# Performance work log

Hardware: AMD Instinct MI355X
Metric: run time of the kernel (lower is better)

The kernel has to match this reference:

```python
import jax, jax.numpy as jnp
import numpy as np
from jax import lax

N = 20000        # nodes
E = 320000       # directed edges (avg degree 16)
F_IN = 512       # input feature dim
HID = 64         # hidden_layer
K_NEI = 8        # sampled neighbors per node
L = K_NEI + 1    # local subgraph size (self + neighbors)
N_TPL = 10       # N_templates
NT = 8           # N_templates_nodes
N_CLS = 6
ALPHA = 0.5      # FGW trade-off
EPS = 0.1        # entropic regularization
N_OUTER = 3      # outer CG iterations
N_SINK = 5       # sinkhorn iterations per outer step


def setup_inputs() -> dict:
    rng = np.random.default_rng(0)
    src = rng.integers(0, N, E).astype(np.int64)
    dst = rng.integers(0, N, E).astype(np.int64)
    edge_index = np.stack([src, dst])

    # fixed-size neighbor table (pad with self, mask)
    nbr = np.full((N, K_NEI), -1, np.int64)
    cnt = np.zeros(N, np.int64)
    for s, d in zip(src, dst):
        c = cnt[s]
        if c < K_NEI:
            nbr[s, c] = d
            cnt[s] = c + 1
    pad = nbr < 0
    self_col = np.arange(N, dtype=np.int64)
    nbr = np.where(pad, self_col[:, None], nbr)
    nbr_mask = np.concatenate([np.ones((N, 1)), (~pad).astype(np.float64)], 1).astype(np.float32)

    # local adjacency among {self, neighbors}: [N, L, L]
    idx_full = np.concatenate([self_col[:, None], nbr], 1)  # [N, L]
    edge_keys = np.unique(src * N + dst)
    keys = idx_full[:, :, None] * N + idx_full[:, None, :]
    C_local = np.isin(keys, edge_keys).astype(np.float32)

    ks = jax.random.split(jax.random.key(0), 10)
    x = jax.random.normal(ks[0], (N, F_IN), jnp.float32)
    W1 = jax.random.normal(ks[1], (F_IN, HID), jnp.float32) / np.float32(np.sqrt(F_IN))
    b1 = jnp.zeros((HID,), jnp.float32)
    W2 = jax.random.normal(ks[2], (HID, HID), jnp.float32) / np.float32(np.sqrt(HID))
    b2 = jnp.zeros((HID,), jnp.float32)
    t = jax.random.uniform(ks[3], (N_TPL, NT, NT), jnp.float32)
    templates = 0.5 * (t + jnp.swapaxes(t, 1, 2))  # symmetric template adjacency
    templates_features = jax.random.normal(ks[4], (N_TPL, NT, HID), jnp.float32)
    Wlin = jax.random.normal(ks[5], (HID + N_TPL, N_CLS), jnp.float32) / np.float32(np.sqrt(HID + N_TPL))
    blin = jnp.zeros((N_CLS,), jnp.float32)
    return {"x": x, "edge_index": jnp.asarray(edge_index), "nbr_idx": jnp.asarray(nbr),
            "nbr_mask": jnp.asarray(nbr_mask), "C_local": jnp.asarray(C_local),
            "W1": W1, "b1": b1, "W2": W2, "b2": b2,
            "templates": templates, "templates_features": templates_features,
            "Wlin": Wlin, "blin": blin}


def gcn(x, W, b, src, dst, n):
    xw = x @ W
    sl = jnp.arange(n)
    s = jnp.concatenate([src, sl])
    d = jnp.concatenate([dst, sl])
    deg = jax.ops.segment_sum(jnp.ones_like(s, jnp.float32), d, num_segments=n)
    dinv = lax.rsqrt(deg)
    coef = dinv[s] * dinv[d]
    return jax.ops.segment_sum(xw[s] * coef[:, None], d, num_segments=n) + b


def fgw_dist(M, C1, h1, C2, h2):
    # entropic fused GW (square loss) with fixed iterations; padded rows have h1 = 0
    f1 = C1 * C1
    f2 = C2 * C2
    constC = (f1 @ h1)[:, None] + (f2 @ h2)[None, :]
    T0 = h1[:, None] * h2[None, :]

    def outer(T, _):
        tens = constC - 2.0 * (C1 @ T @ C2)
        G = (1.0 - ALPHA) * M + ALPHA * tens
        Kmat = jnp.exp(-G / EPS)

        def sink(carry, _):
            u, v = carry
            u = h1 / (Kmat @ v + 1e-16)
            v = h2 / (Kmat.T @ u + 1e-16)
            return (u, v), None

        (u, v), _ = lax.scan(sink, (jnp.ones_like(h1), jnp.ones_like(h2)), None, length=N_SINK)
        return u[:, None] * Kmat * v[None, :], None

    T, _ = lax.scan(outer, T0, None, length=N_OUTER)
    tens = constC - 2.0 * (C1 @ T @ C2)
    return jnp.sum(T * ((1.0 - ALPHA) * M + ALPHA * tens))


def distance_to_template(x, nbr_idx, nbr_mask, C_local, templates_features, templates):
    n = x.shape[0]
    idx_full = jnp.concatenate([jnp.arange(n)[:, None], nbr_idx], axis=1)  # [N, L]
    xl = x[idx_full]  # [N, L, HID]
    # squared euclidean cost to each template: [N, T, L, NT]
    inner = jnp.einsum('nld,tmd->ntlm', xl, templates_features)
    M = (jnp.sum(xl * xl, -1)[:, None, :, None]
         + jnp.sum(templates_features * templates_features, -1)[None, :, None, :]
         - 2.0 * inner)
    h1 = nbr_mask / jnp.sum(nbr_mask, -1, keepdims=True)  # [N, L]
    h2 = jnp.full((NT,), 1.0 / NT, jnp.float32)

    per_tpl = jax.vmap(fgw_dist, in_axes=(0, None, None, 0, None))
    per_node = jax.vmap(per_tpl, in_axes=(0, 0, 0, None, None))
    return per_node(M, C_local, h1, templates, h2)  # [N, N_TPL]


def reference(x, edge_index, nbr_idx, nbr_mask, C_local, W1, b1, W2, b2,
              templates, templates_features, Wlin, blin):
    src, dst = edge_index[0], edge_index[1]
    n = x.shape[0]
    h = jax.nn.relu(gcn(x, W1, b1, src, dst, n))
    h = gcn(h, W2, b2, src, dst, n)
    y = distance_to_template(h, nbr_idx, nbr_mask, C_local, templates_features, templates)
    out = jnp.concatenate([h, y], axis=1) @ Wlin + blin
    return jax.nn.relu(out)
```

## Files before the change

kernel.cpp:

```cpp
#include <hip/hip_runtime.h>


#define NN   20000
#define EE   320000
#define FIN  512
#define HID  64
#define KNEI 8
#define LSZ  9
#define NTPL 10
#define NTN  8
#define NCLS 6
#define CAP  48

typedef unsigned short bf16_t;
typedef unsigned short us8 __attribute__((ext_vector_type(8)));

__device__ __forceinline__ float b2f(bf16_t u) {
  union { unsigned int i; float f; } v; v.i = ((unsigned int)u) << 16; return v.f;
}
__device__ __forceinline__ bf16_t f2b(float f) {
  union { float f; unsigned int i; } v; v.f = f;
  unsigned int x = v.i;
  return (bf16_t)((x + 0x7fffu + ((x >> 16) & 1u)) >> 16);
}
__device__ __forceinline__ float ldf(const void* p, long i, int fp32) {
  return fp32 ? ((const float*)p)[i] : b2f(((const bf16_t*)p)[i]);
}
__device__ __forceinline__ int ldi(const void* p, long i, int i64) {
  return i64 ? (int)((const long long*)p)[i] : ((const int*)p)[i];
}
__device__ __forceinline__ float frcp(float x) { return __builtin_amdgcn_rcpf(x); }

__global__ __launch_bounds__(128) void probe_kernel(const void* __restrict__ x,
                                                    const void* __restrict__ ei,
                                                    const void* __restrict__ tfeat,
                                                    int* __restrict__ flags,
                                                    float* __restrict__ tn2min) {
  __shared__ int sfl[2];
  __shared__ float tn2s[80];
  int tid = threadIdx.x;
  if (tid == 0) {
    int sane = 0;
    for (int k = 0; k < 64; k += 2) {
      bf16_t u = ((const bf16_t*)x)[k];
      int e = (u >> 7) & 0xff;
      if (e >= 112 && e <= 142) sane++;
    }
    int f0 = (sane < 24) ? 1 : 0;
    int zc = 0;
    for (int k = 1; k < 64; k += 2)
      if (((const int*)ei)[k] == 0) zc++;
    int f1 = (zc >= 16) ? 1 : 0;
    flags[0] = f0; flags[1] = f1;
    sfl[0] = f0; sfl[1] = f1;
  }
  __syncthreads();
  if (tid < 80) {
    int fF = sfl[0];
    float s = 0.f;
    for (int k = 0; k < HID; ++k) {
      float v = ldf(tfeat, (long)tid * HID + k, fF);
      s += v * v;
    }
    tn2s[tid] = s;
  }
  __syncthreads();
  if (tid == 0) {
    float gmin = 1e30f;
    for (int t = 0; t < NTPL; ++t) {
      float m = tn2s[t * 8];
      for (int r = 1; r < 8; ++r) m = fminf(m, tn2s[t * 8 + r]);
      tn2min[t] = m;
      gmin = fminf(gmin, m);
    }
    tn2min[NTPL] = gmin;
  }
}

__global__ __launch_bounds__(256) void hist_kernel(const void* __restrict__ ei,
                                                   int* __restrict__ cnt,
                                                   const int* __restrict__ flags) {
  int i = blockIdx.x * 256 + threadIdx.x;
  if (i < EE) atomicAdd(&cnt[ldi(ei, (long)EE + i, flags[1])], 1);
}
__global__ __launch_bounds__(256) void dinv_kernel(const int* __restrict__ cnt,
                                                   float* __restrict__ dinv) {
  int i = blockIdx.x * 256 + threadIdx.x;
  if (i < NN) dinv[i] = rsqrtf((float)cnt[i] + 1.0f);
}

__global__ __launch_bounds__(256) void scatter_kernel(const void* __restrict__ ei,
                                                      int* __restrict__ pos,
                                                      int* __restrict__ slot,
                                                      const int* __restrict__ flags) {
  int i = blockIdx.x * 256 + threadIdx.x;
  if (i >= EE) return;
  int i64 = flags[1];
  int s = ldi(ei, i, i64);
  int d = ldi(ei, (long)EE + i, i64);
  int p = atomicAdd(&pos[d], 1);
  if (p < CAP) slot[d * CAP + p] = s;
}

__global__ __launch_bounds__(256) void gemm1_kernel(const void* __restrict__ x,
                                                    const void* __restrict__ W1,
                                                    float* __restrict__ xw1,
                                                    const int* __restrict__ flags) {
  int wave = blockIdx.x * 4 + (threadIdx.x >> 6);
  int lane = threadIdx.x & 63;
  int row0 = wave * 4;
  if (row0 >= NN) return;
  float a0 = 0.f, a1 = 0.f, a2 = 0.f, a3 = 0.f;
  if (!flags[0]) {
    const bf16_t* xb = (const bf16_t*)x + (long)row0 * FIN;
    const bf16_t* wp = (const bf16_t*)W1;
#pragma unroll 2
    for (int k8 = 0; k8 < FIN / 8; ++k8) {
      us8 r0 = *(const us8*)(xb + k8 * 8);
      us8 r1 = *(const us8*)(xb + FIN + k8 * 8);
      us8 r2 = *(const us8*)(xb + 2 * FIN + k8 * 8);
      us8 r3 = *(const us8*)(xb + 3 * FIN + k8 * 8);
#pragma unroll
      for (int q = 0; q < 8; ++q) {
        float w = b2f(wp[(k8 * 8 + q) * HID + lane]);
        a0 += b2f(r0[q]) * w;
        a1 += b2f(r1[q]) * w;
        a2 += b2f(r2[q]) * w;
        a3 += b2f(r3[q]) * w;
      }
    }
  } else {
    const float* x0 = (const float*)x + (long)row0 * FIN;
    const float* wp = (const float*)W1;
#pragma unroll 8
    for (int k = 0; k < FIN; ++k) {
      float w = wp[k * HID + lane];
      a0 += x0[k] * w;
      a1 += x0[FIN + k] * w;
      a2 += x0[2 * FIN + k] * w;
      a3 += x0[3 * FIN + k] * w;
    }
  }
  xw1[(long)(row0 + 0) * HID + lane] = a0;
  xw1[(long)(row0 + 1) * HID + lane] = a1;
  xw1[(long)(row0 + 2) * HID + lane] = a2;
  xw1[(long)(row0 + 3) * HID + lane] = a3;
}

__global__ __launch_bounds__(256) void gemm2_kernel(const float* __restrict__ h,
                                                    const void* __restrict__ W2,
                                                    float* __restrict__ xw2,
                                                    const int* __restrict__ flags) {
  int wave = blockIdx.x * 4 + (threadIdx.x >> 6);
  int lane = threadIdx.x & 63;
  int row0 = wave * 4;
  if (row0 >= NN) return;
  int fF = flags[0];
  float a0 = 0.f, a1 = 0.f, a2 = 0.f, a3 = 0.f;
  const float* h0 = h + (long)row0 * HID;
#pragma unroll 4
  for (int k4 = 0; k4 < HID / 4; ++k4) {
    float4 r0 = *(const float4*)(h0 + k4 * 4);
    float4 r1 = *(const float4*)(h0 + HID + k4 * 4);
    float4 r2 = *(const float4*)(h0 + 2 * HID + k4 * 4);
    float4 r3 = *(const float4*)(h0 + 3 * HID + k4 * 4);
#pragma unroll
    for (int q = 0; q < 4; ++q) {
      float w = ldf(W2, (k4 * 4 + q) * HID + lane, fF);
      float e0 = (q == 0) ? r0.x : (q == 1) ? r0.y : (q == 2) ? r0.z : r0.w;
      float e1 = (q == 0) ? r1.x : (q == 1) ? r1.y : (q == 2) ? r1.z : r1.w;
      float e2 = (q == 0) ? r2.x : (q == 1) ? r2.y : (q == 2) ? r2.z : r2.w;
      float e3 = (q == 0) ? r3.x : (q == 1) ? r3.y : (q == 2) ? r3.z : r3.w;
      a0 += e0 * w; a1 += e1 * w; a2 += e2 * w; a3 += e3 * w;
    }
  }
  xw2[(long)(row0 + 0) * HID + lane] = a0;
  xw2[(long)(row0 + 1) * HID + lane] = a1;
  xw2[(long)(row0 + 2) * HID + lane] = a2;
  xw2[(long)(row0 + 3) * HID + lane] = a3;
}

__global__ __launch_bounds__(256) void gather_kernel(const float* __restrict__ xw,
                                                     const float* __restrict__ dinv,
                                                     const int* __restrict__ cnt,
                                                     const int* __restrict__ slot,
                                                     float* __restrict__ h,
                                                     const void* __restrict__ bias,
                                                     const int* __restrict__ flags,
                                                     int relu_bias) {
  int n = blockIdx.x * 4 + (threadIdx.x >> 6);
  if (n >= NN) return;
  int c = threadIdx.x & 63;
  float dn = dinv[n];
  float acc = xw[(long)n * HID + c] * dn;
  int m = cnt[n]; if (m > CAP) m = CAP;
  const int* sl = slot + (long)n * CAP;
  int sN = (m > 0) ? sl[0] : 0;
  for (int e = 0; e < m; ++e) {
    int s = sN;
    if (e + 1 < m) sN = sl[e + 1];
    acc += xw[(long)s * HID + c] * dinv[s];
  }
  acc *= dn;
  if (relu_bias) {
    acc += ldf(bias, c, flags[0]);
    acc = acc > 0.f ? acc : 0.f;
  }
  h[(long)n * HID + c] = acc;
}

__global__ __launch_bounds__(256) void norms_kernel(const float* __restrict__ h2,
                                                    const void* __restrict__ b2v,
                                                    float* __restrict__ n2,
                                                    const int* __restrict__ flags) {
  int n = blockIdx.x * 4 + (threadIdx.x >> 6);
  if (n >= NN) return;
  int c = threadIdx.x & 63;
  float v = h2[(long)n * HID + c] + ldf(b2v, c, flags[0]);
  float s = v * v;
  s += __shfl_xor(s, 1); s += __shfl_xor(s, 2); s += __shfl_xor(s, 4);
  s += __shfl_xor(s, 8); s += __shfl_xor(s, 16); s += __shfl_xor(s, 32);
  if (c == 0) n2[n] = s;
}

#define NODES_PB 4
#define TPN 80
#define XLP 65

__global__ __launch_bounds__(320, 2) void fgw_kernel(
    const float* __restrict__ h2,
    const void* __restrict__ b2v,
    const void* __restrict__ nbr_idx,
    const void* __restrict__ nbr_mask,
    const void* __restrict__ C_local,
    const void* __restrict__ tmpl,
    const void* __restrict__ tfeat,
    const void* __restrict__ Wlin,
    const void* __restrict__ blin,
    void* __restrict__ out,
    const int* __restrict__ flags,
    const float* __restrict__ tn2min,
    const float* __restrict__ n2)
{
  const int tid = threadIdx.x;
  const int fF = flags[0];
  const int fI = flags[1];
  const int nb = tid / TPN;
  const int local = tid - nb * TPN;
  const int t = local >> 3;
  const int j = local & 7;
  const int n = blockIdx.x * NODES_PB + nb;
  const int lane = tid & 63;
  const int ob = lane & 56;

  __shared__ float xlS[NODES_PB][LSZ][XLP];
  __shared__ float C1S[NODES_PB][81];
  __shared__ float hwS[NODES_PB][LSZ];
  __shared__ float f1S[NODES_PB][LSZ];
  __shared__ float xnS[NODES_PB][LSZ];
  __shared__ float distS[NODES_PB][NTPL];
  __shared__ float xmaxS[NODES_PB];
  __shared__ int   needS[NODES_PB];
  __shared__ int   sidxS[NODES_PB][LSZ];

  if (local < LSZ) {
    int idx = (local == 0) ? n : ldi(nbr_idx, (long)n * KNEI + local - 1, fI);
    sidxS[nb][local] = idx;
    xnS[nb][local] = n2[idx];
  }
  if (local < HID)
    xlS[nb][0][local] = h2[(long)n * HID + local] + ldf(b2v, local, fF);
  __syncthreads();

  if (local == 0) {
    float xm = xnS[nb][0];
#pragma unroll
    for (int l = 1; l < LSZ; ++l) xm = fmaxf(xm, xnS[nb][l]);
    xmaxS[nb] = xm;
    needS[nb] = ((sqrtf(tn2min[NTPL]) - sqrtf(xm)) >= 5.0990195f) ? 0 : 1;
  }
  __syncthreads();

  const int need = needS[nb];
  if (need) {
    for (int i = local; i < 8 * HID; i += TPN) {
      int l = 1 + (i >> 6), k = i & 63;
      xlS[nb][l][k] = h2[(long)sidxS[nb][l] * HID + k] + ldf(b2v, k, fF);
    }
    for (int i = local; i < 81; i += TPN)
      C1S[nb][i] = ldf(C_local, (long)n * 81 + i, fF);
  }
  __syncthreads();

  if (need && local < LSZ) {
    int l = local;
    float msum = 0.f, f1 = 0.f;
#pragma unroll
    for (int jj = 0; jj < LSZ; ++jj) {
      float mj = ldf(nbr_mask, (long)n * LSZ + jj, fF);
      msum += mj;
      float c = C1S[nb][l * LSZ + jj];
      f1 += c * c * mj;
    }
    float inv = frcp(msum);
    hwS[nb][l] = ldf(nbr_mask, (long)n * LSZ + l, fF) * inv;
    f1S[nb][l] = f1 * inv;
  }
  __syncthreads();

  bool slow = need && ((sqrtf(tn2min[t]) - sqrtf(xmaxS[nb])) < 5.0990195f);
  if (slow) {
    float C2c[NTN];
    float f2h2;
    {
      float s = 0.f;
#pragma unroll
      for (int m = 0; m < NTN; ++m) {
        C2c[m] = ldf(tmpl, t * 64 + m * 8 + j, fF);
        float r = ldf(tmpl, t * 64 + j * 8 + m, fF);
        s += r * r;
      }
      f2h2 = s * 0.125f;
    }
    float hwr[LSZ], f1r[LSZ];
#pragma unroll
    for (int l = 0; l < LSZ; ++l) { hwr[l] = hwS[nb][l]; f1r[l] = f1S[nb][l]; }

    float Mc[LSZ];
    {
      float accI[LSZ];
#pragma unroll
      for (int l = 0; l < LSZ; ++l) accI[l] = 0.f;
      float tn2 = 0.f;
      const long tb = (long)local * HID;
      for (int kb = 0; kb < 8; ++kb) {
        float r[8];
#pragma unroll
        for (int q = 0; q < 8; ++q) r[q] = ldf(tfeat, tb + kb * 8 + q, fF);
#pragma unroll
        for (int q = 0; q < 8; ++q) tn2 += r[q] * r[q];
#pragma unroll
        for (int l = 0; l < LSZ; ++l) {
          float s = 0.f;
#pragma unroll
          for (int q = 0; q < 8; ++q) s += xlS[nb][l][kb * 8 + q] * r[q];
          accI[l] += s;
        }
      }
#pragma unroll
      for (int l = 0; l < LSZ; ++l)
        Mc[l] = xnS[nb][l] + tn2 - 2.f * accI[l];
    }

    float Tc[LSZ], Kc[LSZ], u[LSZ];
#pragma unroll
    for (int l = 0; l < LSZ; ++l) Tc[l] = hwr[l] * 0.125f;

    float v = 1.0f;
    for (int outer = 0; outer < 3; ++outer) {
      float Ac[LSZ];
#pragma unroll
      for (int l = 0; l < LSZ; ++l) {
        float s = 0.f;
#pragma unroll
        for (int l2 = 0; l2 < LSZ; ++l2) s += C1S[nb][l * LSZ + l2] * Tc[l2];
        Ac[l] = s;
      }
#pragma unroll
      for (int l = 0; l < LSZ; ++l) {
        float s = 0.f;
#pragma unroll
        for (int m = 0; m < NTN; ++m) s += __shfl(Ac[l], ob + m) * C2c[m];
        float tens = f1r[l] + f2h2 - 2.f * s;
        Kc[l] = __expf(-5.0f * (Mc[l] + tens));
      }
      v = 1.0f;
      for (int it = 0; it < 5; ++it) {
#pragma unroll
        for (int l = 0; l < LSZ; ++l) {
          float p = Kc[l] * v;
          p += __shfl_xor(p, 1); p += __shfl_xor(p, 2); p += __shfl_xor(p, 4);
          u[l] = hwr[l] * frcp(p + 1e-16f);
        }
        float s = 0.f;
#pragma unroll
        for (int l = 0; l < LSZ; ++l) s += Kc[l] * u[l];
        v = 0.125f * frcp(s + 1e-16f);
      }
#pragma unroll
      for (int l = 0; l < LSZ; ++l) Tc[l] = u[l] * Kc[l] * v;
    }
    {
      float Ac[LSZ];
#pragma unroll
      for (int l = 0; l < LSZ; ++l) {
        float s = 0.f;
#pragma unroll
        for (int l2 = 0; l2 < LSZ; ++l2) s += C1S[nb][l * LSZ + l2] * Tc[l2];
        Ac[l] = s;
      }
      float cl = 0.f;
#pragma unroll
      for (int l = 0; l < LSZ; ++l) {
        float s = 0.f;
#pragma unroll
        for (int m = 0; m < NTN; ++m) s += __shfl(Ac[l], ob + m) * C2c[m];
        float tens = f1r[l] + f2h2 - 2.f * s;
        cl += Tc[l] * 0.5f * (Mc[l] + tens);
      }
      cl += __shfl_xor(cl, 1); cl += __shfl_xor(cl, 2); cl += __shfl_xor(cl, 4);
      if (j == 0) distS[nb][t] = cl;
    }
  } else if (j == 0) {
    distS[nb][t] = 0.f;
  }
  __syncthreads();

  if (local < NCLS) {
    int c = local;
    float acc = ldf(blin, c, fF);
#pragma unroll
    for (int k = 0; k < HID; ++k)
      acc += xlS[nb][0][k] * ldf(Wlin, k * NCLS + c, fF);
#pragma unroll
    for (int tt = 0; tt < NTPL; ++tt)
      acc += distS[nb][tt] * ldf(Wlin, (HID + tt) * NCLS + c, fF);
    float r = acc > 0.f ? acc : 0.f;
    if (fF) ((float*)out)[(long)n * NCLS + c] = r;
    else    ((bf16_t*)out)[(long)n * NCLS + c] = f2b(r);
  }
}

extern "C" void kernel_launch(void* const* d_in, const int* in_sizes, int n_in,
                              void* d_out, int out_size, void* d_ws, size_t ws_size,
                              hipStream_t stream) {
  (void)in_sizes; (void)n_in; (void)out_size; (void)ws_size;
  const void* x     = d_in[0];
  const void* ei    = d_in[1];
  const void* nbr   = d_in[2];
  const void* nmask = d_in[3];
  const void* Cl    = d_in[4];
  const void* W1    = d_in[5];
  const void* b1    = d_in[6];
  const void* W2    = d_in[7];
  const void* b2    = d_in[8];
  const void* tmpl  = d_in[9];
  const void* tfeat = d_in[10];
  const void* Wlin  = d_in[11];
  const void* blin  = d_in[12];

  int*   flags  = (int*)d_ws;
  float* tn2min = (float*)d_ws + 4;
  float* dinv   = (float*)d_ws + 16;
  float* n2     = dinv + NN;
  int*   cnt    = (int*)(n2 + NN);
  int*   pos    = cnt + NN;
  int*   slot   = pos + NN;
  float* bufA   = (float*)(slot + (long)CAP * NN);
  float* bufB   = bufA + (long)NN * HID;

  probe_kernel<<<1, 128, 0, stream>>>(x, ei, tfeat, flags, tn2min);

  hipMemsetAsync(cnt, 0, NN * sizeof(int), stream);
  hipMemsetAsync(pos, 0, NN * sizeof(int), stream);
  hist_kernel<<<(EE + 255) / 256, 256, 0, stream>>>(ei, cnt, flags);
  dinv_kernel<<<(NN + 255) / 256, 256, 0, stream>>>(cnt, dinv);
  scatter_kernel<<<(EE + 255) / 256, 256, 0, stream>>>(ei, pos, slot, flags);

  gemm1_kernel<<<NN / 16, 256, 0, stream>>>(x, W1, bufA, flags);
  gather_kernel<<<NN / 4, 256, 0, stream>>>(bufA, dinv, cnt, slot, bufB,
                                            b1, flags, 1);
  gemm2_kernel<<<NN / 16, 256, 0, stream>>>(bufB, W2, bufA, flags);
  gather_kernel<<<NN / 4, 256, 0, stream>>>(bufA, dinv, cnt, slot, bufB,
                                            b2, flags, 0);

  norms_kernel<<<NN / 4, 256, 0, stream>>>(bufB, b2, n2, flags);

  fgw_kernel<<<NN / NODES_PB, 320, 0, stream>>>(bufB, b2, nbr, nmask, Cl, tmpl,
                                                tfeat, Wlin, blin, d_out, flags,
                                                tn2min, n2);
}
```

Baseline: 343.0 us.

## Use MFMA for first GEMM, drop histogram pass, fuse norms into gather

The first feature GEMM now stages W1 in shared memory in an MFMA-friendly layout and runs bf16 16x16x32 MFMA instructions over 16-row tiles, replacing per-lane scalar FMAs. The separate degree histogram kernel is removed and the atomic position counter from the scatter pass is reused as the in-degree. The norms kernel is fused into the second gather, and gather loads neighbour indices four at a time. This trims launches and redundant passes, but the fp32 fallback path becomes a slow scalar loop and the int4 slot loads read past the count within the CAP-sized row.

New measurement: 480.4 us. +40.0%, slower.

```diff
diff --git a/kernel.cpp b/kernel.cpp
--- a/kernel.cpp
+++ b/kernel.cpp
@@ -14,6 +14,8 @@
 
 typedef unsigned short bf16_t;
 typedef unsigned short us8 __attribute__((ext_vector_type(8)));
+typedef short s16x8 __attribute__((ext_vector_type(8)));
+typedef float f32x4 __attribute__((ext_vector_type(4)));
 
 __device__ __forceinline__ float b2f(bf16_t u) {
   union { unsigned int i; float f; } v; v.i = ((unsigned int)u) << 16; return v.f;
@@ -77,18 +79,6 @@
   }
 }
 
-__global__ __launch_bounds__(256) void hist_kernel(const void* __restrict__ ei,
-                                                   int* __restrict__ cnt,
-                                                   const int* __restrict__ flags) {
-  int i = blockIdx.x * 256 + threadIdx.x;
-  if (i < EE) atomicAdd(&cnt[ldi(ei, (long)EE + i, flags[1])], 1);
-}
-__global__ __launch_bounds__(256) void dinv_kernel(const int* __restrict__ cnt,
-                                                   float* __restrict__ dinv) {
-  int i = blockIdx.x * 256 + threadIdx.x;
-  if (i < NN) dinv[i] = rsqrtf((float)cnt[i] + 1.0f);
-}
-
 __global__ __launch_bounds__(256) void scatter_kernel(const void* __restrict__ ei,
                                                       int* __restrict__ pos,
                                                       int* __restrict__ slot,
@@ -101,50 +91,64 @@
   int p = atomicAdd(&pos[d], 1);
   if (p < CAP) slot[d * CAP + p] = s;
 }
-
-__global__ __launch_bounds__(256) void gemm1_kernel(const void* __restrict__ x,
-                                                    const void* __restrict__ W1,
-                                                    float* __restrict__ xw1,
-                                                    const int* __restrict__ flags) {
-  int wave = blockIdx.x * 4 + (threadIdx.x >> 6);
-  int lane = threadIdx.x & 63;
-  int row0 = wave * 4;
-  if (row0 >= NN) return;
-  float a0 = 0.f, a1 = 0.f, a2 = 0.f, a3 = 0.f;
-  if (!flags[0]) {
-    const bf16_t* xb = (const bf16_t*)x + (long)row0 * FIN;
+__global__ __launch_bounds__(256) void dinv_kernel(const int* __restrict__ cnt,
+                                                   float* __restrict__ dinv) {
+  int i = blockIdx.x * 256 + threadIdx.x;
+  if (i < NN) dinv[i] = rsqrtf((float)cnt[i] + 1.0f);
+}
+
+__global__ __launch_bounds__(256, 2) void gemm1_kernel(const void* __restrict__ x,
+                                                       const void* __restrict__ W1,
+                                                       float* __restrict__ xw1,
+                                                       const int* __restrict__ flags) {
+  __shared__ s16x8 Wf[16][4][64];
+  const int tid = threadIdx.x;
+  const int fF = flags[0];
+  if (!fF) {
     const bf16_t* wp = (const bf16_t*)W1;
-#pragma unroll 2
-    for (int k8 = 0; k8 < FIN / 8; ++k8) {
-      us8 r0 = *(const us8*)(xb + k8 * 8);
-      us8 r1 = *(const us8*)(xb + FIN + k8 * 8);
-      us8 r2 = *(const us8*)(xb + 2 * FIN + k8 * 8);
-      us8 r3 = *(const us8*)(xb + 3 * FIN + k8 * 8);
-#pragma unroll
-      for (int q = 0; q < 8; ++q) {
-        float w = b2f(wp[(k8 * 8 + q) * HID + lane]);
-        a0 += b2f(r0[q]) * w;
-        a1 += b2f(r1[q]) * w;
-        a2 += b2f(r2[q]) * w;
-        a3 += b2f(r3[q]) * w;
-      }
+    for (int idx = tid; idx < FIN * HID; idx += 256) {
+      int k = idx >> 6, n = idx & 63;
+      int kk = k >> 5, q = (k >> 3) & 3, j = k & 7;
+      int nt = n >> 4, m = n & 15;
+      ((bf16_t*)&Wf[kk][nt][q * 16 + m])[j] = wp[idx];
+    }
+  }
+  __syncthreads();
+  const int wid = blockIdx.x * 4 + (tid >> 6);
+  const int lane = tid & 63;
+  if (wid >= NN / 16) return;
+  const int row0 = wid * 16;
+  if (!fF) {
+    const bf16_t* xr = (const bf16_t*)x + (long)(row0 + (lane & 15)) * FIN
+                       + (lane >> 4) * 8;
+    f32x4 acc0 = {0.f, 0.f, 0.f, 0.f}, acc1 = acc0, acc2 = acc0, acc3 = acc0;
+#pragma unroll
+    for (int kk = 0; kk < 16; ++kk) {
+      s16x8 a = *(const s16x8*)(xr + kk * 32);
+      acc0 = __builtin_amdgcn_mfma_f32_16x16x32_bf16(a, Wf[kk][0][lane], acc0, 0, 0, 0);
+      acc1 = __builtin_amdgcn_mfma_f32_16x16x32_bf16(a, Wf[kk][1][lane], acc1, 0, 0, 0);
+      acc2 = __builtin_amdgcn_mfma_f32_16x16x32_bf16(a, Wf[kk][2][lane], acc2, 0, 0, 0);
+      acc3 = __builtin_amdgcn_mfma_f32_16x16x32_bf16(a, Wf[kk][3][lane], acc3, 0, 0, 0);
+    }
+    const int rbase = row0 + (lane >> 4) * 4;
+    const int c = lane & 15;
+#pragma unroll
+    for (int r = 0; r < 4; ++r) {
+      float* o = xw1 + (long)(rbase + r) * HID + c;
+      o[0]  = acc0[r];
+      o[16] = acc1[r];
+      o[32] = acc2[r];
+      o[48] = acc3[r];
     }
   } else {
-    const float* x0 = (const float*)x + (long)row0 * FIN;
     const float* wp = (const float*)W1;
-#pragma unroll 8
-    for (int k = 0; k < FIN; ++k) {
-      float w = wp[k * HID + lane];
-      a0 += x0[k] * w;
-      a1 += x0[FIN + k] * w;
-      a2 += x0[2 * FIN + k] * w;
-      a3 += x0[3 * FIN + k] * w;
-    }
-  }
-  xw1[(long)(row0 + 0) * HID + lane] = a0;
-  xw1[(long)(row0 + 1) * HID + lane] = a1;
-  xw1[(long)(row0 + 2) * HID + lane] = a2;
-  xw1[(long)(row0 + 3) * HID + lane] = a3;
+    for (int r = 0; r < 16; ++r) {
+      const float* x0 = (const float*)x + (long)(row0 + r) * FIN;
+      float a = 0.f;
+      for (int k = 0; k < FIN; ++k) a += x0[k] * wp[k * HID + lane];
+      xw1[(long)(row0 + r) * HID + lane] = a;
+    }
+  }
 }
 
 __global__ __launch_bounds__(256) void gemm2_kernel(const float* __restrict__ h,
@@ -185,9 +189,10 @@
                                                      const int* __restrict__ cnt,
                                                      const int* __restrict__ slot,
                                                      float* __restrict__ h,
+                                                     float* __restrict__ n2,
                                                      const void* __restrict__ bias,
                                                      const int* __restrict__ flags,
-                                                     int relu_bias) {
+                                                     int mode) {
   int n = blockIdx.x * 4 + (threadIdx.x >> 6);
   if (n >= NN) return;
   int c = threadIdx.x & 63;
@@ -195,32 +200,27 @@
   float acc = xw[(long)n * HID + c] * dn;
   int m = cnt[n]; if (m > CAP) m = CAP;
   const int* sl = slot + (long)n * CAP;
-  int sN = (m > 0) ? sl[0] : 0;
-  for (int e = 0; e < m; ++e) {
-    int s = sN;
-    if (e + 1 < m) sN = sl[e + 1];
-    acc += xw[(long)s * HID + c] * dinv[s];
+  for (int e0 = 0; e0 < m; e0 += 4) {
+    int4 s4 = *(const int4*)(sl + e0);
+    if (e0 + 0 < m) acc += xw[(long)s4.x * HID + c] * dinv[s4.x];
+    if (e0 + 1 < m) acc += xw[(long)s4.y * HID + c] * dinv[s4.y];
+    if (e0 + 2 < m) acc += xw[(long)s4.z * HID + c] * dinv[s4.z];
+    if (e0 + 3 < m) acc += xw[(long)s4.w * HID + c] * dinv[s4.w];
   }
   acc *= dn;
-  if (relu_bias) {
-    acc += ldf(bias, c, flags[0]);
+  float b = ldf(bias, c, flags[0]);
+  if (mode) {
+    acc += b;
     acc = acc > 0.f ? acc : 0.f;
-  }
-  h[(long)n * HID + c] = acc;
-}
-
-__global__ __launch_bounds__(256) void norms_kernel(const float* __restrict__ h2,
-                                                    const void* __restrict__ b2v,
-                                                    float* __restrict__ n2,
-                                                    const int* __restrict__ flags) {
-  int n = blockIdx.x * 4 + (threadIdx.x >> 6);
-  if (n >= NN) return;
-  int c = threadIdx.x & 63;
-  float v = h2[(long)n * HID + c] + ldf(b2v, c, flags[0]);
-  float s = v * v;
-  s += __shfl_xor(s, 1); s += __shfl_xor(s, 2); s += __shfl_xor(s, 4);
-  s += __shfl_xor(s, 8); s += __shfl_xor(s, 16); s += __shfl_xor(s, 32);
-  if (c == 0) n2[n] = s;
+    h[(long)n * HID + c] = acc;
+  } else {
+    h[(long)n * HID + c] = acc;
+    float v = acc + b;
+    float s = v * v;
+    s += __shfl_xor(s, 1); s += __shfl_xor(s, 2); s += __shfl_xor(s, 4);
+    s += __shfl_xor(s, 8); s += __shfl_xor(s, 16); s += __shfl_xor(s, 32);
+    if (c == 0) n2[n] = s;
+  }
 }
 
 #define NODES_PB 4
@@ -453,28 +453,23 @@
   float* tn2min = (float*)d_ws + 4;
   float* dinv   = (float*)d_ws + 16;
   float* n2     = dinv + NN;
-  int*   cnt    = (int*)(n2 + NN);
-  int*   pos    = cnt + NN;
+  int*   pos    = (int*)(n2 + NN);
   int*   slot   = pos + NN;
   float* bufA   = (float*)(slot + (long)CAP * NN);
   float* bufB   = bufA + (long)NN * HID;
 
   probe_kernel<<<1, 128, 0, stream>>>(x, ei, tfeat, flags, tn2min);
 
-  hipMemsetAsync(cnt, 0, NN * sizeof(int), stream);
   hipMemsetAsync(pos, 0, NN * sizeof(int), stream);
-  hist_kernel<<<(EE + 255) / 256, 256, 0, stream>>>(ei, cnt, flags);
-  dinv_kernel<<<(NN + 255) / 256, 256, 0, stream>>>(cnt, dinv);
   scatter_kernel<<<(EE + 255) / 256, 256, 0, stream>>>(ei, pos, slot, flags);
-
-  gemm1_kernel<<<NN / 16, 256, 0, stream>>>(x, W1, bufA, flags);
-  gather_kernel<<<NN / 4, 256, 0, stream>>>(bufA, dinv, cnt, slot, bufB,
-                                            b1, flags, 1);
+  dinv_kernel<<<(NN + 255) / 256, 256, 0, stream>>>(pos, dinv);
+
+  gemm1_kernel<<<(NN / 16 + 3) / 4, 256, 0, stream>>>(x, W1, bufA, flags);
+  gather_kernel<<<NN / 4, 256, 0, stream>>>(bufA, dinv, pos, slot, bufB,
+                                            n2, b1, flags, 1);
   gemm2_kernel<<<NN / 16, 256, 0, stream>>>(bufB, W2, bufA, flags);
-  gather_kernel<<<NN / 4, 256, 0, stream>>>(bufA, dinv, cnt, slot, bufB,
-                                            b2, flags, 0);
-
-  norms_kernel<<<NN / 4, 256, 0, stream>>>(bufB, b2, n2, flags);
+  gather_kernel<<<NN / 4, 256, 0, stream>>>(bufA, dinv, pos, slot, bufB,
+                                            n2, b2, flags, 0);
 
   fgw_kernel<<<NN / NODES_PB, 320, 0, stream>>>(bufB, b2, nbr, nmask, Cl, tmpl,
                                                 tfeat, Wlin, blin, d_out, flags,
```
